# Kernel optimization log

Measured on AMD Instinct MI355X. Metric: run time of the kernel, lower is better.

The kernel has to match this reference:

```python
import jax, jax.numpy as jnp
import numpy as np

N_NODES = 100000
N_EDGES = 1000000
NODE_F = 128
EDGE_F = 16
HID = 64


def _layernorm(h, g, b, eps=1e-5):
    mu = jnp.mean(h, axis=-1, keepdims=True)
    var = jnp.var(h, axis=-1, keepdims=True)
    return (h - mu) * jax.lax.rsqrt(var + eps) * g + b


def _sage_conv(x, src, dst, Wl, bl, Wr):
    # PyG SAGEConv (aggr='mean'): out = lin_l(mean_{j in N(i)} x_j) + lin_r(x_i)
    agg = jax.ops.segment_sum(x[src], dst, num_segments=N_NODES)
    deg = jax.ops.segment_sum(jnp.ones((src.shape[0], 1), x.dtype), dst, num_segments=N_NODES)
    mean = agg / jnp.maximum(deg, 1.0)
    return mean @ Wl + bl + x @ Wr


def setup_inputs() -> dict:
    key = jax.random.key(0)
    ks = jax.random.split(key, 20)
    def lin(k, fi, fo):
        return jax.random.normal(k, (fi, fo), jnp.float32) / np.sqrt(fi)
    inp = {
        'x': jax.random.normal(ks[0], (N_NODES, NODE_F), jnp.float32),
        'edge_index': jax.random.randint(ks[1], (2, N_EDGES), 0, N_NODES, jnp.int32),
        'edge_attr': jax.random.normal(ks[2], (N_EDGES, EDGE_F), jnp.float32),
        # layer 0
        'Wl0': lin(ks[3], NODE_F, HID), 'bl0': jnp.zeros((HID,), jnp.float32),
        'Wr0': lin(ks[4], NODE_F, HID),
        'g0': jnp.ones((HID,), jnp.float32), 'be0': jnp.zeros((HID,), jnp.float32),
        # layer 1
        'Wl1': lin(ks[5], HID, HID), 'bl1': jnp.zeros((HID,), jnp.float32),
        'Wr1': lin(ks[6], HID, HID),
        'g1': jnp.ones((HID,), jnp.float32), 'be1': jnp.zeros((HID,), jnp.float32),
        # MLP: (2*HID+EDGE_F) -> HID -> HID//2 -> 1
        'W1': lin(ks[7], 2 * HID + EDGE_F, HID), 'b1': jnp.zeros((HID,), jnp.float32),
        'W2': lin(ks[8], HID, HID // 2), 'b2': jnp.zeros((HID // 2,), jnp.float32),
        'W3': lin(ks[9], HID // 2, 1), 'b3': jnp.zeros((1,), jnp.float32),
    }
    return inp


def reference(x, edge_index, edge_attr, Wl0, bl0, Wr0, g0, be0, Wl1, bl1, Wr1, g1, be1, W1, b1, W2, b2, W3, b3):
    src, dst = edge_index[0], edge_index[1]
    # encoder layer 0 (dropout inactive in eval)
    h = jax.nn.relu(_layernorm(_sage_conv(x, src, dst, Wl0, bl0, Wr0), g0, be0))
    # encoder layer 1
    h = jax.nn.relu(_layernorm(_sage_conv(h, src, dst, Wl1, bl1, Wr1), g1, be1))
    # edge representation: [src_emb | dst_emb | edge_attr]
    edge_repr = jnp.concatenate([h[src], h[dst], edge_attr], axis=-1)
    z = jax.nn.relu(edge_repr @ W1 + b1)
    z = jax.nn.relu(z @ W2 + b2)
    return (z @ W3 + b3).squeeze(-1)
```

## Files before the change

### kernel.cpp

```cpp
#include <hip/hip_runtime.h>
#include <hip/hip_bf16.h>

#define NN 100000
#define NE 1000000

typedef _Float16 half8  __attribute__((ext_vector_type(8)));
typedef float    f32x4  __attribute__((ext_vector_type(4)));

__device__ inline unsigned int pk2(float a, float b) {
    auto h = __builtin_amdgcn_cvt_pkrtz(a, b);
    return __builtin_bit_cast(unsigned int, h);
}
__device__ inline float f16lo(unsigned int u) {
    return (float)__builtin_bit_cast(_Float16, (unsigned short)(u & 0xffffu));
}
__device__ inline float f16hi(unsigned int u) {
    return (float)__builtin_bit_cast(_Float16, (unsigned short)(u >> 16));
}

__global__ __launch_bounds__(256) void deg_int_kernel(const int* __restrict__ dst, int* __restrict__ degi) {
    int e = blockIdx.x * 256 + threadIdx.x;
    if (e < NE) atomicAdd(&degi[dst[e]], 1);
}

__global__ __launch_bounds__(256) void scan_partial(const int* __restrict__ degi, int* __restrict__ bs) {
    __shared__ int sd[256];
    int b = blockIdx.x, t = threadIdx.x;
    int i = b * 512 + t;
    int v = (i < NN ? degi[i] : 0) + (i + 256 < NN ? degi[i + 256] : 0);
    sd[t] = v;
    __syncthreads();
    for (int o = 128; o > 0; o >>= 1) {
        if (t < o) sd[t] += sd[t + o];
        __syncthreads();
    }
    if (t == 0) bs[b] = sd[0];
}

__global__ __launch_bounds__(256) void scan_spine(const int* __restrict__ bs, int* __restrict__ bo) {
    __shared__ int sd[256];
    int t = threadIdx.x;
    int v = (t < 196) ? bs[t] : 0;
    sd[t] = v;
    __syncthreads();
    for (int o = 1; o < 256; o <<= 1) {
        int add = (t >= o) ? sd[t - o] : 0;
        __syncthreads();
        sd[t] += add;
        __syncthreads();
    }
    if (t < 196) bo[t] = sd[t] - v;
}

__global__ __launch_bounds__(512) void scan_final(const int* __restrict__ degi, const int* __restrict__ bo,
                                                  int* __restrict__ offs, int* __restrict__ cursor) {
    __shared__ int sd[512];
    int b = blockIdx.x, t = threadIdx.x;
    int i = b * 512 + t;
    int v = (i < NN) ? degi[i] : 0;
    sd[t] = v;
    __syncthreads();
    for (int o = 1; o < 512; o <<= 1) {
        int add = (t >= o) ? sd[t - o] : 0;
        __syncthreads();
        sd[t] += add;
        __syncthreads();
    }
    if (i < NN) {
        int ex = bo[b] + sd[t] - v;
        offs[i] = ex;
        cursor[i] = ex;
    }
}

__global__ __launch_bounds__(256) void csr_fill(const int* __restrict__ src, const int* __restrict__ dst,
                                                int* __restrict__ cursor, int* __restrict__ csr) {
    int e = blockIdx.x * 256 + threadIdx.x;
    if (e < NE) {
        int pos = atomicAdd(&cursor[dst[e]], 1);
        csr[pos] = src[e];
    }
}

template <int K, bool INF16>
__global__ __launch_bounds__(256, 1) void gemm_node(const void* __restrict__ inp,
                                                    const float* __restrict__ WL,
                                                    const float* __restrict__ WR,
                                                    _Float16* __restrict__ outP) {
    __shared__ __align__(16) _Float16 wt[128 * K];
    __shared__ __align__(16) _Float16 at[4][16 * 128];

    int tid = threadIdx.x;
    for (int i = tid; i < K * 64; i += 256) {
        int k = i >> 6, n = i & 63;
        wt[n * K + k]        = (_Float16)WL[i];
        wt[(64 + n) * K + k] = (_Float16)WR[i];
    }
    __syncthreads();

    int wave = tid >> 6, lane = tid & 63;
    int g = lane >> 4, r = lane & 15;

    half8 bf[8][K / 32];
#pragma unroll
    for (int nt = 0; nt < 8; ++nt)
#pragma unroll
        for (int ks = 0; ks < K / 32; ++ks)
            bf[nt][ks] = *(const half8*)&wt[(nt * 16 + r) * K + ks * 32 + g * 8];

    int rowbase = blockIdx.x * 64 + wave * 16;
    int eq = lane >> 2, qq = lane & 3;
    int srow = rowbase + eq;
    if (srow > NN - 1) srow = NN - 1;
    _Float16* A = &at[wave][0];

    if constexpr (!INF16) {
        const float* sr = (const float*)inp + (size_t)srow * K + qq * (K / 4);
        unsigned int pk[K / 8];
#pragma unroll
        for (int i = 0; i < K / 16; ++i) {
            float4 v = ((const float4*)sr)[i];
            pk[2 * i]     = pk2(v.x, v.y);
            pk[2 * i + 1] = pk2(v.z, v.w);
        }
        unsigned int* da = (unsigned int*)(A + eq * K + qq * (K / 4));
#pragma unroll
        for (int i = 0; i < K / 32; ++i)
            ((uint4*)da)[i] = make_uint4(pk[4 * i], pk[4 * i + 1], pk[4 * i + 2], pk[4 * i + 3]);
    } else {
        const _Float16* sr = (const _Float16*)inp + (size_t)srow * K + qq * (K / 4);
        uint4* da = (uint4*)(A + eq * K + qq * (K / 4));
#pragma unroll
        for (int i = 0; i < K / 32; ++i)
            da[i] = ((const uint4*)sr)[i];
    }

    f32x4 acc[8];
#pragma unroll
    for (int nt = 0; nt < 8; ++nt) acc[nt] = f32x4{0.f, 0.f, 0.f, 0.f};
#pragma unroll
    for (int ks = 0; ks < K / 32; ++ks) {
        half8 af = *(const half8*)(A + r * K + ks * 32 + g * 8);
#pragma unroll
        for (int nt = 0; nt < 8; ++nt)
            acc[nt] = __builtin_amdgcn_mfma_f32_16x16x32_f16(af, bf[nt][ks], acc[nt], 0, 0, 0);
    }

#pragma unroll
    for (int nt = 0; nt < 8; ++nt)
#pragma unroll
        for (int rr = 0; rr < 4; ++rr)
            A[(g * 4 + rr) * 128 + nt * 16 + r] = (_Float16)acc[nt][rr];
    __syncthreads();
#pragma unroll
    for (int it = 0; it < 2; ++it) {
        int lrow = it * 8 + (lane >> 3);
        int cc = (lane & 7) * 16;
        int grow = rowbase + lrow;
        if (grow < NN) {
            uint4 u0 = *(const uint4*)&A[lrow * 128 + cc];
            uint4 u1 = *(const uint4*)&A[lrow * 128 + cc + 8];
            *(uint4*)&outP[(size_t)grow * 128 + cc] = u0;
            *(uint4*)&outP[(size_t)grow * 128 + cc + 8] = u1;
        }
    }
}

__global__ __launch_bounds__(256) void gather_f16(const _Float16* __restrict__ v, const int* __restrict__ csr,
                                                  const int* __restrict__ offs, const int* __restrict__ degi,
                                                  float* __restrict__ agg) {
    int tid = threadIdx.x;
    int node = blockIdx.x * 4 + (tid >> 6);
    int lane = tid & 63;
    if (node >= NN) return;
    int h0 = lane >> 5, c = lane & 31;
    int off = offs[node], cnt = degi[node];
    float a0 = 0.f, a1 = 0.f;
    int j = 0;
    for (; j + 4 <= cnt; j += 4) {
        int r0 = csr[off + j + h0];
        int r1 = csr[off + j + 2 + h0];
        unsigned int u0 = *(const unsigned int*)&v[(size_t)r0 * 128 + 2 * c];
        unsigned int u1 = *(const unsigned int*)&v[(size_t)r1 * 128 + 2 * c];
        a0 += f16lo(u0); a1 += f16hi(u0);
        a0 += f16lo(u1); a1 += f16hi(u1);
    }
    for (; j + 2 <= cnt; j += 2) {
        int r0 = csr[off + j + h0];
        unsigned int u0 = *(const unsigned int*)&v[(size_t)r0 * 128 + 2 * c];
        a0 += f16lo(u0); a1 += f16hi(u0);
    }
    if (j < cnt && h0 == 0) {
        int r0 = csr[off + j];
        unsigned int u0 = *(const unsigned int*)&v[(size_t)r0 * 128 + 2 * c];
        a0 += f16lo(u0); a1 += f16hi(u0);
    }
    a0 += __shfl_xor(a0, 32, 64);
    a1 += __shfl_xor(a1, 32, 64);
    if (h0 == 0) {
        float2 o; o.x = a0; o.y = a1;
        *(float2*)&agg[(size_t)node * 64 + 2 * c] = o;
    }
}

__global__ __launch_bounds__(256) void ln_elem(const float* __restrict__ agg, const int* __restrict__ degi,
                                               const _Float16* __restrict__ proj,
                                               const float* __restrict__ bl, const float* __restrict__ g,
                                               const float* __restrict__ be, _Float16* __restrict__ out) {
    int tid = threadIdx.x;
    int wave = tid >> 6, lane = tid & 63;
    int h0 = lane >> 5, c = lane & 31;
    int node = blockIdx.x * 8 + wave * 2 + h0;
    if (node >= NN) return;
    unsigned int up = *(const unsigned int*)&proj[(size_t)node * 128 + 64 + 2 * c];
    float p0 = f16lo(up), p1 = f16hi(up);
    float2 ag = *(const float2*)&agg[(size_t)node * 64 + 2 * c];
    float dg = (float)degi[node];
    dg = dg < 1.f ? 1.f : dg;
    float v0 = ag.x / dg + bl[2 * c] + p0;
    float v1 = ag.y / dg + bl[2 * c + 1] + p1;
    float s = v0 + v1, s2 = v0 * v0 + v1 * v1;
#pragma unroll
    for (int o = 16; o > 0; o >>= 1) {
        s  += __shfl_xor(s, o, 64);
        s2 += __shfl_xor(s2, o, 64);
    }
    float mu = s * (1.f / 64.f);
    float var = s2 * (1.f / 64.f) - mu * mu;
    float rs = rsqrtf(var + 1e-5f);
    float h0v = (v0 - mu) * rs * g[2 * c] + be[2 * c];
    float h1v = (v1 - mu) * rs * g[2 * c + 1] + be[2 * c + 1];
    h0v = h0v > 0.f ? h0v : 0.f;
    h1v = h1v > 0.f ? h1v : 0.f;
    *(unsigned int*)&out[(size_t)node * 64 + 2 * c] = pk2(h0v, h1v);
}

#define NTILES 15625
__global__ __launch_bounds__(256) void edge_mlp_mfma(const _Float16* __restrict__ h,
                                                     const int* __restrict__ src,
                                                     const int* __restrict__ dst,
                                                     const float* __restrict__ ea,
                                                     const float* __restrict__ W1,
                                                     const float* __restrict__ b1,
                                                     const float* __restrict__ W2,
                                                     const float* __restrict__ b2,
                                                     const float* __restrict__ W3,
                                                     const float* __restrict__ b3,
                                                     float* __restrict__ out) {
    __shared__ __align__(16) _Float16 w1t[64 * 160];
    __shared__ __align__(16) _Float16 w2t[32 * 64];
    __shared__ __align__(16) _Float16 atile[4][16 * 160];
    __shared__ __align__(16) _Float16 z1t[4][16 * 72];

    int tid = threadIdx.x;
    for (int i = tid; i < 64 * 160 / 2; i += 256) ((unsigned int*)w1t)[i] = 0u;
    __syncthreads();
    for (int i = tid; i < 144 * 64; i += 256) {
        int k = i >> 6, n = i & 63;
        w1t[n * 160 + k] = (_Float16)W1[i];
    }
    for (int i = tid; i < 64 * 32; i += 256) {
        int k = i >> 5, n = i & 31;
        w2t[n * 64 + k] = (_Float16)W2[i];
    }
    __syncthreads();

    int wave = tid >> 6;
    int lane = tid & 63;
    int g = lane >> 4;
    int r = lane & 15;

    half8 b1f[4][5];
#pragma unroll
    for (int nt = 0; nt < 4; ++nt)
#pragma unroll
        for (int ks = 0; ks < 5; ++ks)
            b1f[nt][ks] = *(const half8*)&w1t[(nt * 16 + r) * 160 + ks * 32 + g * 8];
    half8 b2f[2][2];
#pragma unroll
    for (int nt = 0; nt < 2; ++nt)
#pragma unroll
        for (int ks = 0; ks < 2; ++ks)
            b2f[nt][ks] = *(const half8*)&w2t[(nt * 16 + r) * 64 + ks * 32 + g * 8];

    float b1c0 = b1[0 * 16 + r], b1c1 = b1[1 * 16 + r], b1c2 = b1[2 * 16 + r], b1c3 = b1[3 * 16 + r];
    float b2c0 = b2[0 * 16 + r], b2c1 = b2[1 * 16 + r];
    float w3c0 = W3[0 * 16 + r], w3c1 = W3[1 * 16 + r];
    float b3v = b3[0];

    _Float16* A = &atile[wave][0];
    _Float16* Z = &z1t[wave][0];
    int eq = lane >> 2;
    int qq = lane & 3;

    for (int t = blockIdx.x; t < NTILES; t += gridDim.x) {
        int ebase = t * 64 + wave * 16;
        int e = ebase + eq;
        int s = src[e];
        int d = dst[e];

        const _Float16* srow = (qq < 2) ? (h + (size_t)s * 64 + qq * 32)
                                        : (h + (size_t)d * 64 + (qq - 2) * 32);
        uint4* da = (uint4*)(A + eq * 160 + qq * 32);
#pragma unroll
        for (int i = 0; i < 4; ++i) da[i] = ((const uint4*)srow)[i];
        float4 av = *(const float4*)(ea + (size_t)e * 16 + qq * 4);
        uint2 eapk; eapk.x = pk2(av.x, av.y); eapk.y = pk2(av.z, av.w);
        *(uint2*)(A + eq * 160 + 128 + qq * 4) = eapk;
        uint2 zz; zz.x = 0u; zz.y = 0u;
        *(uint2*)(A + eq * 160 + 144 + qq * 4) = zz;

        f32x4 c1_0 = {b1c0, b1c0, b1c0, b1c0};
        f32x4 c1_1 = {b1c1, b1c1, b1c1, b1c1};
        f32x4 c1_2 = {b1c2, b1c2, b1c2, b1c2};
        f32x4 c1_3 = {b1c3, b1c3, b1c3, b1c3};
#pragma unroll
        for (int ks = 0; ks < 5; ++ks) {
            half8 af = *(const half8*)(A + r * 160 + ks * 32 + g * 8);
            c1_0 = __builtin_amdgcn_mfma_f32_16x16x32_f16(af, b1f[0][ks], c1_0, 0, 0, 0);
            c1_1 = __builtin_amdgcn_mfma_f32_16x16x32_f16(af, b1f[1][ks], c1_1, 0, 0, 0);
            c1_2 = __builtin_amdgcn_mfma_f32_16x16x32_f16(af, b1f[2][ks], c1_2, 0, 0, 0);
            c1_3 = __builtin_amdgcn_mfma_f32_16x16x32_f16(af, b1f[3][ks], c1_3, 0, 0, 0);
        }
#pragma unroll
        for (int rr = 0; rr < 4; ++rr) {
            float v0 = c1_0[rr]; v0 = v0 > 0.f ? v0 : 0.f;
            float v1 = c1_1[rr]; v1 = v1 > 0.f ? v1 : 0.f;
            float v2 = c1_2[rr]; v2 = v2 > 0.f ? v2 : 0.f;
            float v3 = c1_3[rr]; v3 = v3 > 0.f ? v3 : 0.f;
            int row = g * 4 + rr;
            Z[row * 72 + 0 * 16 + r] = (_Float16)v0;
            Z[row * 72 + 1 * 16 + r] = (_Float16)v1;
            Z[row * 72 + 2 * 16 + r] = (_Float16)v2;
            Z[row * 72 + 3 * 16 + r] = (_Float16)v3;
        }

        f32x4 c2_0 = {b2c0, b2c0, b2c0, b2c0};
        f32x4 c2_1 = {b2c1, b2c1, b2c1, b2c1};
#pragma unroll
        for (int ks = 0; ks < 2; ++ks) {
            half8 a2 = *(const half8*)(Z + r * 72 + ks * 32 + g * 8);
            c2_0 = __builtin_amdgcn_mfma_f32_16x16x32_f16(a2, b2f[0][ks], c2_0, 0, 0, 0);
            c2_1 = __builtin_amdgcn_mfma_f32_16x16x32_f16(a2, b2f[1][ks], c2_1, 0, 0, 0);
        }

        float t0, t1, t2, t3;
        {
            float u0, u1;
            u0 = c2_0[0]; u0 = u0 > 0.f ? u0 : 0.f;
            u1 = c2_1[0]; u1 = u1 > 0.f ? u1 : 0.f;
            t0 = u0 * w3c0 + u1 * w3c1;
            u0 = c2_0[1]; u0 = u0 > 0.f ? u0 : 0.f;
            u1 = c2_1[1]; u1 = u1 > 0.f ? u1 : 0.f;
            t1 = u0 * w3c0 + u1 * w3c1;
            u0 = c2_0[2]; u0 = u0 > 0.f ? u0 : 0.f;
            u1 = c2_1[2]; u1 = u1 > 0.f ? u1 : 0.f;
            t2 = u0 * w3c0 + u1 * w3c1;
            u0 = c2_0[3]; u0 = u0 > 0.f ? u0 : 0.f;
            u1 = c2_1[3]; u1 = u1 > 0.f ? u1 : 0.f;
            t3 = u0 * w3c0 + u1 * w3c1;
        }
#pragma unroll
        for (int m = 1; m < 16; m <<= 1) {
            t0 += __shfl_xor(t0, m, 64);
            t1 += __shfl_xor(t1, m, 64);
            t2 += __shfl_xor(t2, m, 64);
            t3 += __shfl_xor(t3, m, 64);
        }
        if (r == 0) out[ebase + g * 4 + 0] = t0 + b3v;
        if (r == 1) out[ebase + g * 4 + 1] = t1 + b3v;
        if (r == 2) out[ebase + g * 4 + 2] = t2 + b3v;
        if (r == 3) out[ebase + g * 4 + 3] = t3 + b3v;
    }
}

#define WS_AGG   0
#define WS_BUFP  25600000
#define WS_BUFH  51200000
#define WS_DEGI  64000000
#define WS_OFFS  64400000
#define WS_CSR   64800000
#define WS_NEED  68800000

extern "C" void kernel_launch(void* const* d_in, const int* in_sizes, int n_in,
                              void* d_out, int out_size, void* d_ws, size_t ws_size,
                              hipStream_t stream) {
    const float* x   = (const float*)d_in[0];
    const int*   ei  = (const int*)d_in[1];
    const float* ea  = (const float*)d_in[2];
    const float* Wl0 = (const float*)d_in[3];
    const float* bl0 = (const float*)d_in[4];
    const float* Wr0 = (const float*)d_in[5];
    const float* g0  = (const float*)d_in[6];
    const float* be0 = (const float*)d_in[7];
    const float* Wl1 = (const float*)d_in[8];
    const float* bl1 = (const float*)d_in[9];
    const float* Wr1 = (const float*)d_in[10];
    const float* g1  = (const float*)d_in[11];
    const float* be1 = (const float*)d_in[12];
    const float* W1  = (const float*)d_in[13];
    const float* b1  = (const float*)d_in[14];
    const float* W2  = (const float*)d_in[15];
    const float* b2  = (const float*)d_in[16];
    const float* W3  = (const float*)d_in[17];
    const float* b3  = (const float*)d_in[18];
    float* out = (float*)d_out;

    const int* src  = ei;
    const int* dstp = ei + NE;

    char* ws = (char*)d_ws;
    float*     agg  = (float*)(ws + WS_AGG);
    _Float16*  bufP = (_Float16*)(ws + WS_BUFP);
    _Float16*  bufH = (_Float16*)(ws + WS_BUFH);
    int*       degi = (int*)(ws + WS_DEGI);
    int*       offs = (int*)(ws + WS_OFFS);
    int*       csr  = (int*)(ws + WS_CSR);
    int*       cursor = (int*)(ws + WS_AGG);
    int*       bsum   = (int*)(ws + WS_BUFP);
    int*       boff   = (int*)(ws + WS_BUFP + 4096);

    hipMemsetAsync(degi, 0, 400000, stream);
    deg_int_kernel<<<(NE + 255) / 256, 256, 0, stream>>>(dstp, degi);
    scan_partial<<<196, 256, 0, stream>>>(degi, bsum);
    scan_spine<<<1, 256, 0, stream>>>(bsum, boff);
    scan_final<<<196, 512, 0, stream>>>(degi, boff, offs, cursor);
    csr_fill<<<(NE + 255) / 256, 256, 0, stream>>>(src, dstp, cursor, csr);

    const int gemm_grid = (NN + 63) / 64;
    gemm_node<128, false><<<gemm_grid, 256, 0, stream>>>(x, Wl0, Wr0, bufP);
    gather_f16<<<NN / 4, 256, 0, stream>>>(bufP, csr, offs, degi, agg);
    ln_elem<<<(NN + 7) / 8, 256, 0, stream>>>(agg, degi, bufP, bl0, g0, be0, bufH);

    gemm_node<64, true><<<gemm_grid, 256, 0, stream>>>(bufH, Wl1, Wr1, bufP);
    gather_f16<<<NN / 4, 256, 0, stream>>>(bufP, csr, offs, degi, agg);
    ln_elem<<<(NN + 7) / 8, 256, 0, stream>>>(agg, degi, bufP, bl1, g1, be1, bufH);

    edge_mlp_mfma<<<3125, 256, 0, stream>>>(bufH, src, dstp, ea,
                                            W1, b1, W2, b2, W3, b3, out);
}
```

Baseline: 589.0 us.

## Fuse gather with layernorm, split projection buffers, pad LDS strides

Merges the neighbor-mean gather and the layernorm/ReLU kernel into one, so the fp32 aggregate buffer is no longer written and read back. The node GEMM now writes the neighbor projection and the self projection into two separate 64-wide fp16 arrays, which makes the gathered rows contiguous and halves their stride. LDS row strides are padded (136 and 168) to reduce bank conflicts, and edge_mlp shares one LDS buffer between the weight staging and the per-wave tiles, lowering LDS use. The risk is that the gather kernel now carries extra registers and the layernorm tail, and the second gemm_node reads and writes bufH in sequence, which relies on kernel ordering.

```diff
diff --git a/kernel.cpp b/kernel.cpp
--- a/kernel.cpp
+++ b/kernel.cpp
@@ -86,9 +86,10 @@
 __global__ __launch_bounds__(256, 1) void gemm_node(const void* __restrict__ inp,
                                                     const float* __restrict__ WL,
                                                     const float* __restrict__ WR,
-                                                    _Float16* __restrict__ outP) {
+                                                    _Float16* __restrict__ outL,
+                                                    _Float16* __restrict__ outR) {
     __shared__ __align__(16) _Float16 wt[128 * K];
-    __shared__ __align__(16) _Float16 at[4][16 * 128];
+    __shared__ __align__(16) _Float16 at[4][16 * 136];
 
     int tid = threadIdx.x;
     for (int i = tid; i < K * 64; i += 256) {
@@ -123,13 +124,13 @@
             pk[2 * i]     = pk2(v.x, v.y);
             pk[2 * i + 1] = pk2(v.z, v.w);
         }
-        unsigned int* da = (unsigned int*)(A + eq * K + qq * (K / 4));
+        unsigned int* da = (unsigned int*)(A + eq * 136 + qq * (K / 4));
 #pragma unroll
         for (int i = 0; i < K / 32; ++i)
             ((uint4*)da)[i] = make_uint4(pk[4 * i], pk[4 * i + 1], pk[4 * i + 2], pk[4 * i + 3]);
     } else {
         const _Float16* sr = (const _Float16*)inp + (size_t)srow * K + qq * (K / 4);
-        uint4* da = (uint4*)(A + eq * K + qq * (K / 4));
+        uint4* da = (uint4*)(A + eq * 136 + qq * (K / 4));
 #pragma unroll
         for (int i = 0; i < K / 32; ++i)
             da[i] = ((const uint4*)sr)[i];
@@ -140,7 +141,7 @@
     for (int nt = 0; nt < 8; ++nt) acc[nt] = f32x4{0.f, 0.f, 0.f, 0.f};
 #pragma unroll
     for (int ks = 0; ks < K / 32; ++ks) {
-        half8 af = *(const half8*)(A + r * K + ks * 32 + g * 8);
+        half8 af = *(const half8*)(A + r * 136 + ks * 32 + g * 8);
 #pragma unroll
         for (int nt = 0; nt < 8; ++nt)
             acc[nt] = __builtin_amdgcn_mfma_f32_16x16x32_f16(af, bf[nt][ks], acc[nt], 0, 0, 0);
@@ -150,7 +151,7 @@
     for (int nt = 0; nt < 8; ++nt)
 #pragma unroll
         for (int rr = 0; rr < 4; ++rr)
-            A[(g * 4 + rr) * 128 + nt * 16 + r] = (_Float16)acc[nt][rr];
+            A[(g * 4 + rr) * 136 + nt * 16 + r] = (_Float16)acc[nt][rr];
     __syncthreads();
 #pragma unroll
     for (int it = 0; it < 2; ++it) {
@@ -158,17 +159,28 @@
         int cc = (lane & 7) * 16;
         int grow = rowbase + lrow;
         if (grow < NN) {
-            uint4 u0 = *(const uint4*)&A[lrow * 128 + cc];
-            uint4 u1 = *(const uint4*)&A[lrow * 128 + cc + 8];
-            *(uint4*)&outP[(size_t)grow * 128 + cc] = u0;
-            *(uint4*)&outP[(size_t)grow * 128 + cc + 8] = u1;
-        }
-    }
-}
-
-__global__ __launch_bounds__(256) void gather_f16(const _Float16* __restrict__ v, const int* __restrict__ csr,
-                                                  const int* __restrict__ offs, const int* __restrict__ degi,
-                                                  float* __restrict__ agg) {
+            uint4 u0 = *(const uint4*)&A[lrow * 136 + cc];
+            uint4 u1 = *(const uint4*)&A[lrow * 136 + cc + 8];
+            if (cc < 64) {
+                *(uint4*)&outL[(size_t)grow * 64 + cc] = u0;
+                *(uint4*)&outL[(size_t)grow * 64 + cc + 8] = u1;
+            } else {
+                *(uint4*)&outR[(size_t)grow * 64 + cc - 64] = u0;
+                *(uint4*)&outR[(size_t)grow * 64 + cc - 56] = u1;
+            }
+        }
+    }
+}
+
+__global__ __launch_bounds__(256) void gather_ln(const _Float16* __restrict__ vL,
+                                                 const _Float16* __restrict__ pR,
+                                                 const int* __restrict__ csr,
+                                                 const int* __restrict__ offs,
+                                                 const int* __restrict__ degi,
+                                                 const float* __restrict__ bl,
+                                                 const float* __restrict__ g,
+                                                 const float* __restrict__ be,
+                                                 _Float16* __restrict__ out) {
     int tid = threadIdx.x;
     int node = blockIdx.x * 4 + (tid >> 6);
     int lane = tid & 63;
@@ -180,45 +192,30 @@
     for (; j + 4 <= cnt; j += 4) {
         int r0 = csr[off + j + h0];
         int r1 = csr[off + j + 2 + h0];
-        unsigned int u0 = *(const unsigned int*)&v[(size_t)r0 * 128 + 2 * c];
-        unsigned int u1 = *(const unsigned int*)&v[(size_t)r1 * 128 + 2 * c];
+        unsigned int u0 = *(const unsigned int*)&vL[(size_t)r0 * 64 + 2 * c];
+        unsigned int u1 = *(const unsigned int*)&vL[(size_t)r1 * 64 + 2 * c];
         a0 += f16lo(u0); a1 += f16hi(u0);
         a0 += f16lo(u1); a1 += f16hi(u1);
     }
     for (; j + 2 <= cnt; j += 2) {
         int r0 = csr[off + j + h0];
-        unsigned int u0 = *(const unsigned int*)&v[(size_t)r0 * 128 + 2 * c];
+        unsigned int u0 = *(const unsigned int*)&vL[(size_t)r0 * 64 + 2 * c];
         a0 += f16lo(u0); a1 += f16hi(u0);
     }
     if (j < cnt && h0 == 0) {
         int r0 = csr[off + j];
-        unsigned int u0 = *(const unsigned int*)&v[(size_t)r0 * 128 + 2 * c];
+        unsigned int u0 = *(const unsigned int*)&vL[(size_t)r0 * 64 + 2 * c];
         a0 += f16lo(u0); a1 += f16hi(u0);
     }
     a0 += __shfl_xor(a0, 32, 64);
     a1 += __shfl_xor(a1, 32, 64);
-    if (h0 == 0) {
-        float2 o; o.x = a0; o.y = a1;
-        *(float2*)&agg[(size_t)node * 64 + 2 * c] = o;
-    }
-}
-
-__global__ __launch_bounds__(256) void ln_elem(const float* __restrict__ agg, const int* __restrict__ degi,
-                                               const _Float16* __restrict__ proj,
-                                               const float* __restrict__ bl, const float* __restrict__ g,
-                                               const float* __restrict__ be, _Float16* __restrict__ out) {
-    int tid = threadIdx.x;
-    int wave = tid >> 6, lane = tid & 63;
-    int h0 = lane >> 5, c = lane & 31;
-    int node = blockIdx.x * 8 + wave * 2 + h0;
-    if (node >= NN) return;
-    unsigned int up = *(const unsigned int*)&proj[(size_t)node * 128 + 64 + 2 * c];
-    float p0 = f16lo(up), p1 = f16hi(up);
-    float2 ag = *(const float2*)&agg[(size_t)node * 64 + 2 * c];
-    float dg = (float)degi[node];
+
+    float dg = (float)cnt;
     dg = dg < 1.f ? 1.f : dg;
-    float v0 = ag.x / dg + bl[2 * c] + p0;
-    float v1 = ag.y / dg + bl[2 * c + 1] + p1;
+    float2 blv = *(const float2*)&bl[2 * c];
+    unsigned int up = *(const unsigned int*)&pR[(size_t)node * 64 + 2 * c];
+    float v0 = a0 / dg + blv.x + f16lo(up);
+    float v1 = a1 / dg + blv.y + f16hi(up);
     float s = v0 + v1, s2 = v0 * v0 + v1 * v1;
 #pragma unroll
     for (int o = 16; o > 0; o >>= 1) {
@@ -228,14 +225,17 @@
     float mu = s * (1.f / 64.f);
     float var = s2 * (1.f / 64.f) - mu * mu;
     float rs = rsqrtf(var + 1e-5f);
-    float h0v = (v0 - mu) * rs * g[2 * c] + be[2 * c];
-    float h1v = (v1 - mu) * rs * g[2 * c + 1] + be[2 * c + 1];
+    float2 gv  = *(const float2*)&g[2 * c];
+    float2 bev = *(const float2*)&be[2 * c];
+    float h0v = (v0 - mu) * rs * gv.x + bev.x;
+    float h1v = (v1 - mu) * rs * gv.y + bev.y;
     h0v = h0v > 0.f ? h0v : 0.f;
     h1v = h1v > 0.f ? h1v : 0.f;
-    *(unsigned int*)&out[(size_t)node * 64 + 2 * c] = pk2(h0v, h1v);
+    if (h0 == 0) *(unsigned int*)&out[(size_t)node * 64 + 2 * c] = pk2(h0v, h1v);
 }
 
 #define NTILES 15625
+#define ASTR 168
 __global__ __launch_bounds__(256) void edge_mlp_mfma(const _Float16* __restrict__ h,
                                                      const int* __restrict__ src,
                                                      const int* __restrict__ dst,
@@ -247,10 +247,9 @@
                                                      const float* __restrict__ W3,
                                                      const float* __restrict__ b3,
                                                      float* __restrict__ out) {
-    __shared__ __align__(16) _Float16 w1t[64 * 160];
-    __shared__ __align__(16) _Float16 w2t[32 * 64];
-    __shared__ __align__(16) _Float16 atile[4][16 * 160];
-    __shared__ __align__(16) _Float16 z1t[4][16 * 72];
+    __shared__ __align__(16) char smem[30720];
+    _Float16* w1t = (_Float16*)smem;
+    _Float16* w2t = (_Float16*)(smem + 20480);
 
     int tid = threadIdx.x;
     for (int i = tid; i < 64 * 160 / 2; i += 256) ((unsigned int*)w1t)[i] = 0u;
@@ -282,14 +281,16 @@
 #pragma unroll
         for (int ks = 0; ks < 2; ++ks)
             b2f[nt][ks] = *(const half8*)&w2t[(nt * 16 + r) * 64 + ks * 32 + g * 8];
+    __syncthreads();
+
+    _Float16* A = (_Float16*)(smem + wave * (16 * ASTR * 2));
+    _Float16* Z = (_Float16*)(smem + 4 * (16 * ASTR * 2) + wave * (16 * 72 * 2));
 
     float b1c0 = b1[0 * 16 + r], b1c1 = b1[1 * 16 + r], b1c2 = b1[2 * 16 + r], b1c3 = b1[3 * 16 + r];
     float b2c0 = b2[0 * 16 + r], b2c1 = b2[1 * 16 + r];
     float w3c0 = W3[0 * 16 + r], w3c1 = W3[1 * 16 + r];
     float b3v = b3[0];
 
-    _Float16* A = &atile[wave][0];
-    _Float16* Z = &z1t[wave][0];
     int eq = lane >> 2;
     int qq = lane & 3;
 
@@ -301,14 +302,14 @@
 
         const _Float16* srow = (qq < 2) ? (h + (size_t)s * 64 + qq * 32)
                                         : (h + (size_t)d * 64 + (qq - 2) * 32);
-        uint4* da = (uint4*)(A + eq * 160 + qq * 32);
+        uint4* da = (uint4*)(A + eq * ASTR + qq * 32);
 #pragma unroll
         for (int i = 0; i < 4; ++i) da[i] = ((const uint4*)srow)[i];
         float4 av = *(const float4*)(ea + (size_t)e * 16 + qq * 4);
         uint2 eapk; eapk.x = pk2(av.x, av.y); eapk.y = pk2(av.z, av.w);
-        *(uint2*)(A + eq * 160 + 128 + qq * 4) = eapk;
+        *(uint2*)(A + eq * ASTR + 128 + qq * 4) = eapk;
         uint2 zz; zz.x = 0u; zz.y = 0u;
-        *(uint2*)(A + eq * 160 + 144 + qq * 4) = zz;
+        *(uint2*)(A + eq * ASTR + 144 + qq * 4) = zz;
 
         f32x4 c1_0 = {b1c0, b1c0, b1c0, b1c0};
         f32x4 c1_1 = {b1c1, b1c1, b1c1, b1c1};
@@ -316,7 +317,7 @@
         f32x4 c1_3 = {b1c3, b1c3, b1c3, b1c3};
 #pragma unroll
         for (int ks = 0; ks < 5; ++ks) {
-            half8 af = *(const half8*)(A + r * 160 + ks * 32 + g * 8);
+            half8 af = *(const half8*)(A + r * ASTR + ks * 32 + g * 8);
             c1_0 = __builtin_amdgcn_mfma_f32_16x16x32_f16(af, b1f[0][ks], c1_0, 0, 0, 0);
             c1_1 = __builtin_amdgcn_mfma_f32_16x16x32_f16(af, b1f[1][ks], c1_1, 0, 0, 0);
             c1_2 = __builtin_amdgcn_mfma_f32_16x16x32_f16(af, b1f[2][ks], c1_2, 0, 0, 0);
@@ -374,13 +375,15 @@
     }
 }
 
-#define WS_AGG   0
-#define WS_BUFP  25600000
-#define WS_BUFH  51200000
-#define WS_DEGI  64000000
-#define WS_OFFS  64400000
-#define WS_CSR   64800000
-#define WS_NEED  68800000
+#define WS_PROJL  0
+#define WS_PROJR  12800000
+#define WS_BUFH   25600000
+#define WS_DEGI   38400000
+#define WS_OFFS   38800000
+#define WS_CSR    39200000
+#define WS_CURS   43200000
+#define WS_BSUM   43600000
+#define WS_BOFF   43604096
 
 extern "C" void kernel_launch(void* const* d_in, const int* in_sizes, int n_in,
                               void* d_out, int out_size, void* d_ws, size_t ws_size,
@@ -410,15 +413,15 @@
     const int* dstp = ei + NE;
 
     char* ws = (char*)d_ws;
-    float*     agg  = (float*)(ws + WS_AGG);
-    _Float16*  bufP = (_Float16*)(ws + WS_BUFP);
-    _Float16*  bufH = (_Float16*)(ws + WS_BUFH);
-    int*       degi = (int*)(ws + WS_DEGI);
-    int*       offs = (int*)(ws + WS_OFFS);
-    int*       csr  = (int*)(ws + WS_CSR);
-    int*       cursor = (int*)(ws + WS_AGG);
-    int*       bsum   = (int*)(ws + WS_BUFP);
-    int*       boff   = (int*)(ws + WS_BUFP + 4096);
+    _Float16* projL = (_Float16*)(ws + WS_PROJL);
+    _Float16* projR = (_Float16*)(ws + WS_PROJR);
+    _Float16* bufH  = (_Float16*)(ws + WS_BUFH);
+    int* degi   = (int*)(ws + WS_DEGI);
+    int* offs   = (int*)(ws + WS_OFFS);
+    int* csr    = (int*)(ws + WS_CSR);
+    int* cursor = (int*)(ws + WS_CURS);
+    int* bsum   = (int*)(ws + WS_BSUM);
+    int* boff   = (int*)(ws + WS_BOFF);
 
     hipMemsetAsync(degi, 0, 400000, stream);
     deg_int_kernel<<<(NE + 255) / 256, 256, 0, stream>>>(dstp, degi);
@@ -428,13 +431,11 @@
     csr_fill<<<(NE + 255) / 256, 256, 0, stream>>>(src, dstp, cursor, csr);
 
     const int gemm_grid = (NN + 63) / 64;
-    gemm_node<128, false><<<gemm_grid, 256, 0, stream>>>(x, Wl0, Wr0, bufP);
-    gather_f16<<<NN / 4, 256, 0, stream>>>(bufP, csr, offs, degi, agg);
-    ln_elem<<<(NN + 7) / 8, 256, 0, stream>>>(agg, degi, bufP, bl0, g0, be0, bufH);
-
-    gemm_node<64, true><<<gemm_grid, 256, 0, stream>>>(bufH, Wl1, Wr1, bufP);
-    gather_f16<<<NN / 4, 256, 0, stream>>>(bufP, csr, offs, degi, agg);
-    ln_elem<<<(NN + 7) / 8, 256, 0, stream>>>(agg, degi, bufP, bl1, g1, be1, bufH);
+    gemm_node<128, false><<<gemm_grid, 256, 0, stream>>>(x, Wl0, Wr0, projL, projR);
+    gather_ln<<<NN / 4, 256, 0, stream>>>(projL, projR, csr, offs, degi, bl0, g0, be0, bufH);
+
+    gemm_node<64, true><<<gemm_grid, 256, 0, stream>>>(bufH, Wl1, Wr1, projL, projR);
+    gather_ln<<<NN / 4, 256, 0, stream>>>(projL, projR, csr, offs, degi, bl1, g1, be1, bufH);
 
     edge_mlp_mfma<<<3125, 256, 0, stream>>>(bufH, src, dstp, ea,
                                             W1, b1, W2, b2, W3, b3, out);
```

Result: no change. 586.1 us (-0.5%).
